# Kernel optimization log

Hardware: AMD Instinct MI355X
Metric: run time of the kernel (lower is better)

## Reference

```python
import jax, jax.numpy as jnp
import numpy as np

H = 8          # n_heads
M = 16         # max_dist
U = 512        # n_units
DH = U // H    # d_head
EPS = 1e-3     # keras LayerNormalization default epsilon
NEG = -2.0**32 + 1.0


def _rel_table(pe, T):
    # pe: [2M+1, DH]; returns [T, T, DH] with rel[i, j] = pe[clip(j - i, -M, M) + M]
    i = jnp.arange(T)
    idx = jnp.clip(i[None, :] - i[:, None], -M, M) + M
    return pe[idx]


def _split_heads(x):
    # [B, T, U] -> [H*B, T, DH]  (head-major, matching tf.concat(tf.split(x, H, 2), 0))
    B, T, _ = x.shape
    return x.reshape(B, T, H, DH).transpose(2, 0, 1, 3).reshape(H * B, T, DH)


def _merge_heads(x, B):
    # [H*B, T, DH] -> [B, T, U]
    T = x.shape[1]
    return x.reshape(H, B, T, DH).transpose(1, 2, 0, 3).reshape(B, T, U)


def setup_inputs() -> dict:
    key = jax.random.key(0)
    ks = jax.random.split(key, 10)
    B, T = 8, 1024
    s = 1.0 / np.sqrt(U)
    inp = {
        'q': jax.random.normal(ks[0], (B, T, U), jnp.float32),
        'k': jax.random.normal(ks[1], (B, T, U), jnp.float32),
        'v': jax.random.normal(ks[2], (B, T, U), jnp.float32),
        'Wq': jax.random.normal(ks[3], (U, U), jnp.float32) * s,
        'bq': jnp.zeros((U,), jnp.float32),
        'Wk': jax.random.normal(ks[4], (U, U), jnp.float32) * s,
        'bk': jnp.zeros((U,), jnp.float32),
        'Wv': jax.random.normal(ks[5], (U, U), jnp.float32) * s,
        'bv': jnp.zeros((U,), jnp.float32),
        'Wo': jax.random.normal(ks[6], (U, U), jnp.float32) * s,
        'bo': jnp.zeros((U,), jnp.float32),
        'gamma': jnp.ones((U,), jnp.float32),
        'beta': jnp.zeros((U,), jnp.float32),
        'pe_k': jax.random.normal(ks[7], (2 * M + 1, DH), jnp.float32) * 0.05,
        'pe_v': jax.random.normal(ks[8], (2 * M + 1, DH), jnp.float32) * 0.05,
    }
    return inp


def reference(q, k, v, Wq, bq, Wk, bk, Wv, bv, Wo, bo, gamma, beta, pe_k, pe_v):
    B, T, _ = q.shape
    relu = jax.nn.relu
    q_emb = relu(q @ Wq + bq)
    k_emb = relu(k @ Wk + bk)
    v_emb = relu(v @ Wv + bv)
    qh = _split_heads(q_emb)   # [HB, T, DH]
    kh = _split_heads(k_emb)
    vh = _split_heads(v_emb)

    attn = jnp.einsum('btd,bsd->bts', qh, kh)
    rel_k = _rel_table(pe_k, T)                       # [T, T, DH]
    attn = attn + jnp.einsum('btd,tsd->bts', qh, rel_k)
    attn = attn / jnp.asarray(DH, attn.dtype) ** 0.5

    causal = jnp.tril(jnp.ones((T, T), jnp.bool_))
    attn = jnp.where(causal[None], attn, jnp.asarray(NEG, attn.dtype))
    w = jax.nn.softmax(attn, axis=-1)

    out = jnp.einsum('bts,bsd->btd', w, vh)
    rel_v = _rel_table(pe_v, T)
    out = out + jnp.einsum('bts,tsd->btd', w, rel_v)

    out = _merge_heads(out, B)                        # [B, T, U]
    out = relu(out @ Wo + bo)
    out = out + q

    mu = jnp.mean(out, axis=-1, keepdims=True)
    var = jnp.mean(jnp.square(out - mu), axis=-1, keepdims=True)
    return (out - mu) * jax.lax.rsqrt(var + EPS) * gamma + beta
```

## Files before the change

### kernel.cpp

```cpp
#include <hip/hip_runtime.h>
#include <hip/hip_bf16.h>

#define T_SEQ 1024
#define U_DIM 512
#define LN_EPS 1e-3f

typedef float  f32x4  __attribute__((ext_vector_type(4)));
typedef short  bf16x8 __attribute__((ext_vector_type(8)));

__device__ __forceinline__ unsigned short f2bf(float f) {
    union { float f; unsigned u; } x; x.f = f;
    unsigned r = x.u + 0x7fffu + ((x.u >> 16) & 1u);
    return (unsigned short)(r >> 16);
}
__device__ __forceinline__ float b2f(short s) {
    union { unsigned u; float f; } x; x.u = ((unsigned)(unsigned short)s) << 16;
    return x.f;
}
__device__ __forceinline__ int packbf(float a, float b) {
    return (int)((unsigned)f2bf(a) | ((unsigned)f2bf(b) << 16));
}
__device__ __forceinline__ void async_copy16(void* lds, const void* g) {
    __builtin_amdgcn_global_load_lds((const __attribute__((address_space(1))) void*)g,
                                     (__attribute__((address_space(3))) void*)lds, 16, 0, 0);
}

__global__ __launch_bounds__(256) void conv_bf16(
        const float* __restrict__ q, const float* __restrict__ k, const float* __restrict__ v,
        short* __restrict__ qb, short* __restrict__ kb, short* __restrict__ vb) {
    const size_t off = ((size_t)blockIdx.x * 256 + threadIdx.x) * 8;
#pragma unroll
    for (int z = 0; z < 3; ++z) {
        const float* src = (z == 0) ? q : (z == 1) ? k : v;
        short* dst = (z == 0) ? qb : (z == 1) ? kb : vb;
        float4 a = *(const float4*)(src + off);
        float4 b = *(const float4*)(src + off + 4);
        int4 o;
        o.x = packbf(a.x, a.y);
        o.y = packbf(a.z, a.w);
        o.z = packbf(b.x, b.y);
        o.w = packbf(b.z, b.w);
        *(int4*)(dst + off) = o;
    }
}

__global__ __launch_bounds__(256) void prep_wt(
        const float* __restrict__ Wq, const float* __restrict__ Wk,
        const float* __restrict__ Wv, const float* __restrict__ Wo,
        short* __restrict__ wt) {
    __shared__ float Ws[64][65];
    const int bid = blockIdx.x, t = threadIdx.x;
    const int z = bid >> 6, tile = bid & 63;
    const float* W = (z == 0) ? Wq : (z == 1) ? Wk : (z == 2) ? Wv : Wo;
    short* Wt = wt + (size_t)z * 262144;
    const int k0 = (tile >> 3) * 64, n0 = (tile & 7) * 64;
    {
        const int kr = t >> 2, cs = (t & 3) * 16;
        const float4* src = (const float4*)(W + (size_t)(k0 + kr) * 512 + n0 + cs);
#pragma unroll
        for (int i = 0; i < 4; ++i) {
            float4 vv = src[i];
            Ws[kr][cs + 4 * i + 0] = vv.x;
            Ws[kr][cs + 4 * i + 1] = vv.y;
            Ws[kr][cs + 4 * i + 2] = vv.z;
            Ws[kr][cs + 4 * i + 3] = vv.w;
        }
    }
    __syncthreads();
    {
        const int nr = t >> 2, ks = (t & 3) * 16;
        int4 w0, w1;
        w0.x = packbf(Ws[ks + 0][nr], Ws[ks + 1][nr]);
        w0.y = packbf(Ws[ks + 2][nr], Ws[ks + 3][nr]);
        w0.z = packbf(Ws[ks + 4][nr], Ws[ks + 5][nr]);
        w0.w = packbf(Ws[ks + 6][nr], Ws[ks + 7][nr]);
        w1.x = packbf(Ws[ks + 8][nr], Ws[ks + 9][nr]);
        w1.y = packbf(Ws[ks + 10][nr], Ws[ks + 11][nr]);
        w1.z = packbf(Ws[ks + 12][nr], Ws[ks + 13][nr]);
        w1.w = packbf(Ws[ks + 14][nr], Ws[ks + 15][nr]);
        short* dst = Wt + (size_t)(n0 + nr) * 512 + k0 + ks;
        *(int4*)dst = w0;
        *(int4*)(dst + 8) = w1;
    }
}

template <int OUT, int BM, int BN>
__global__ __launch_bounds__(256) void gemm_mfma(
        const void* __restrict__ A0, const void* __restrict__ A1, const void* __restrict__ A2,
        const short* __restrict__ Wt0, const short* __restrict__ Wt1, const short* __restrict__ Wt2,
        const float* __restrict__ b0p, const float* __restrict__ b1p, const float* __restrict__ b2p,
        const float* __restrict__ resid,
        void* __restrict__ O0, void* __restrict__ O1, void* __restrict__ O2) {
    constexpr int ASZ = BM * 64;
    constexpr int BSZ = BN * 64;
    constexpr int MW  = BM / 64;
    constexpr int NW  = 4 / MW;
    constexpr int AJ  = BN / (16 * NW);
    constexpr int BNC = BN / 16;
    constexpr int NTW = BNC / 2;
    constexpr int ACB = BM / 32;
    __shared__ short As[2 * ASZ];
    __shared__ short Bs[2 * BSZ];

    const int z = blockIdx.z;
    const void* Av = (z == 0) ? A0 : (z == 1) ? A1 : A2;
    const short* Wz = (z == 0) ? Wt0 : (z == 1) ? Wt1 : Wt2;
    const float* bz = (z == 0) ? b0p : (z == 1) ? b1p : b2p;
    void* Ov = (z == 0) ? O0 : (z == 1) ? O1 : O2;

    const int tid = threadIdx.x;
    const int m0 = blockIdx.x * BM, n0 = blockIdx.y * BN;
    const int w = tid >> 6, lane = tid & 63;
    const int n15 = lane & 15, g = lane >> 4;
    const int mh = w / NW, nh = w % NW;

    f32x4 acc[4][AJ];
#pragma unroll
    for (int i = 0; i < 4; ++i)
#pragma unroll
        for (int j = 0; j < AJ; ++j) acc[i][j] = (f32x4){0.f, 0.f, 0.f, 0.f};

#define STAGE_B(CK, BUF)                                                                 \
    do {                                                                                 \
        if (w < 2) {                                                                     \
            _Pragma("unroll")                                                            \
            for (int i = 0; i < 2 * NTW; ++i) {                                          \
                const int kc = i / NTW, nt = w * NTW + (i % NTW);                        \
                const short* gp = Wz + (size_t)(n0 + nt * 16 + n15) * 512 + (CK) * 64 + kc * 32 + g * 8; \
                async_copy16(Bs + (BUF) * BSZ + (kc * BNC + nt) * 512, gp);              \
            }                                                                            \
        }                                                                                \
    } while (0)

#define STAGE_A(CK, BUF)                                                                 \
    do {                                                                                 \
        if (w >= 2) {                                                                    \
            _Pragma("unroll")                                                            \
            for (int i = 0; i < 2 * ACB; ++i) {                                          \
                const int kc = i / ACB, mt = (w - 2) * ACB + (i % ACB);                  \
                const short* gp = (const short*)Av + (size_t)(m0 + mt * 16 + n15) * 512 + (CK) * 64 + kc * 32 + g * 8; \
                async_copy16(As + (BUF) * ASZ + (kc * (BM / 16) + mt) * 512, gp);        \
            }                                                                            \
        }                                                                                \
    } while (0)

    STAGE_B(0, 0);
    STAGE_A(0, 0);

    for (int ck = 0; ck < 8; ++ck) {
        const int cb = ck & 1, nb = cb ^ 1;
        __syncthreads();
        if (ck < 7) {
            STAGE_B(ck + 1, nb);
            STAGE_A(ck + 1, nb);
        }
#pragma unroll
        for (int kc = 0; kc < 2; ++kc) {
            bf16x8 af[4], bfv[AJ];
#pragma unroll
            for (int i = 0; i < 4; ++i)
                af[i] = *(const bf16x8*)(As + cb * ASZ + (kc * (BM / 16) + mh * 4 + i) * 512 + lane * 8);
#pragma unroll
            for (int j = 0; j < AJ; ++j)
                bfv[j] = *(const bf16x8*)(Bs + cb * BSZ + (kc * BNC + nh * AJ + j) * 512 + lane * 8);
#pragma unroll
            for (int i = 0; i < 4; ++i)
#pragma unroll
                for (int j = 0; j < AJ; ++j)
                    acc[i][j] = __builtin_amdgcn_mfma_f32_16x16x32_bf16(af[i], bfv[j], acc[i][j], 0, 0, 0);
        }
    }
#undef STAGE_B
#undef STAGE_A

    const int mbase = m0 + mh * 64 + g * 4;
    const int nbase = n0 + nh * (AJ * 16) + n15;
    const bool even = (n15 & 1) == 0;
    float bj[AJ];
#pragma unroll
    for (int j = 0; j < AJ; ++j) bj[j] = bz[nbase + j * 16];

#pragma unroll
    for (int i = 0; i < 4; ++i) {
        const int mrow = mbase + i * 16;
#pragma unroll
        for (int j = 0; j < AJ; ++j) {
            const int ncol = nbase + j * 16;
            f32x4 a = acc[i][j];
            float v0 = fmaxf(a[0] + bj[j], 0.f);
            float v1 = fmaxf(a[1] + bj[j], 0.f);
            float v2 = fmaxf(a[2] + bj[j], 0.f);
            float v3 = fmaxf(a[3] + bj[j], 0.f);
            if (OUT == 0) {
                unsigned t01 = (unsigned)packbf(v0, v1);
                unsigned t23 = (unsigned)packbf(v2, v3);
                unsigned x01 = (unsigned)__shfl_xor((int)t01, 1, 64);
                unsigned x23 = (unsigned)__shfl_xor((int)t23, 1, 64);
                short* Oz = (short*)Ov;
                if (even) {
                    unsigned d0 = (t01 & 0xffffu) | (x01 << 16);
                    unsigned d1 = (t01 >> 16) | (x01 & 0xffff0000u);
                    *(unsigned*)(Oz + (size_t)(mrow + 0) * 512 + ncol) = d0;
                    *(unsigned*)(Oz + (size_t)(mrow + 1) * 512 + ncol) = d1;
                } else {
                    unsigned d2 = (x23 & 0xffffu) | (t23 << 16);
                    unsigned d3 = (x23 >> 16) | (t23 & 0xffff0000u);
                    *(unsigned*)(Oz + (size_t)(mrow + 2) * 512 + ncol - 1) = d2;
                    *(unsigned*)(Oz + (size_t)(mrow + 3) * 512 + ncol - 1) = d3;
                }
            } else {
                float x0 = __shfl_xor(v0, 1, 64);
                float x1 = __shfl_xor(v1, 1, 64);
                float x2 = __shfl_xor(v2, 1, 64);
                float x3 = __shfl_xor(v3, 1, 64);
                float* Oz = (float*)Ov;
                if (even) {
                    float2 r0 = *(const float2*)(resid + (size_t)(mrow + 0) * 512 + ncol);
                    float2 r1 = *(const float2*)(resid + (size_t)(mrow + 1) * 512 + ncol);
                    *(float2*)(Oz + (size_t)(mrow + 0) * 512 + ncol) = make_float2(v0 + r0.x, x0 + r0.y);
                    *(float2*)(Oz + (size_t)(mrow + 1) * 512 + ncol) = make_float2(v1 + r1.x, x1 + r1.y);
                } else {
                    float2 r2 = *(const float2*)(resid + (size_t)(mrow + 2) * 512 + ncol - 1);
                    float2 r3 = *(const float2*)(resid + (size_t)(mrow + 3) * 512 + ncol - 1);
                    *(float2*)(Oz + (size_t)(mrow + 2) * 512 + ncol - 1) = make_float2(x2 + r2.x, v2 + r2.y);
                    *(float2*)(Oz + (size_t)(mrow + 3) * 512 + ncol - 1) = make_float2(x3 + r3.x, v3 + r3.y);
                }
            }
        }
    }
}

__global__ __launch_bounds__(256) void attn_mfma(
        const short* __restrict__ qe, const short* __restrict__ ke,
        const short* __restrict__ ve, const float* __restrict__ pe_k,
        float* __restrict__ ml, short* __restrict__ ao) {
    __shared__ short Kc[2 * 4096];
    __shared__ short Vc[2 * 4096];
    __shared__ float qpeS[4 * 16 * 17];

    const int tid = threadIdx.x;
    const int bid = blockIdx.x;
    const int rank = (bid & 3) + 4 * (bid >> 8);
    const int hb = (bid >> 2) & 63;
    const int tt = 15 - rank;
    const int h = hb >> 3, b = hb & 7;
    const int w = tid >> 6, lane = tid & 63;
    const int g = lane >> 4, n15 = lane & 15;
    const int sp = tid & 31, dbase = (tid >> 5) * 8;
    float* qpeW = qpeS + w * (16 * 17);

    const size_t rowbase = (size_t)b * T_SEQ;

    int qn = 0;
    bf16x8 Bq[2];
    float qpe0 = 0.f;
    float m_r = -3.0e38f, l_r = 0.f;
    f32x4 oacc[4];

#define SETUP(TILE)                                                                      \
    do {                                                                                 \
        qn = (TILE) * 64 + w * 16;                                                       \
        _Pragma("unroll")                                                                \
        for (int kh = 0; kh < 2; ++kh)                                                   \
            Bq[kh] = *(const bf16x8*)(qe + (rowbase + qn + n15) * U_DIM + h * 64 + kh * 32 + g * 8); \
        f32x4 qa[2];                                                                     \
        qa[0] = (f32x4){0.f, 0.f, 0.f, 0.f};                                             \
        qa[1] = (f32x4){0.f, 0.f, 0.f, 0.f};                                             \
        _Pragma("unroll")                                                                \
        for (int mt = 0; mt < 2; ++mt)                                                   \
        _Pragma("unroll")                                                                \
        for (int kh = 0; kh < 2; ++kh) {                                                 \
            const float* src = pe_k + (mt * 16 + n15) * 64 + kh * 32 + g * 8;            \
            float4 f0 = *(const float4*)src;                                             \
            float4 f1 = *(const float4*)(src + 4);                                       \
            bf16x8 fr;                                                                   \
            fr[0] = (short)f2bf(f0.x); fr[1] = (short)f2bf(f0.y);                        \
            fr[2] = (short)f2bf(f0.z); fr[3] = (short)f2bf(f0.w);                        \
            fr[4] = (short)f2bf(f1.x); fr[5] = (short)f2bf(f1.y);                        \
            fr[6] = (short)f2bf(f1.z); fr[7] = (short)f2bf(f1.w);                        \
            qa[mt] = __builtin_amdgcn_mfma_f32_16x16x32_bf16(fr, Bq[kh], qa[mt], 0, 0, 0); \
        }                                                                                \
        _Pragma("unroll")                                                                \
        for (int mt = 0; mt < 2; ++mt)                                                   \
        _Pragma("unroll")                                                                \
        for (int r = 0; r < 4; ++r) {                                                    \
            const int ri = mt * 16 + 4 * g + r;                                          \
            if (ri <= 16) qpeW[n15 * 17 + ri] = qa[mt][r];                               \
        }                                                                                \
        qpe0 = qpeW[n15 * 17];                                                           \
        m_r = -3.0e38f; l_r = 0.f;                                                       \
        _Pragma("unroll")                                                                \
        for (int dt = 0; dt < 4; ++dt) oacc[dt] = (f32x4){0.f, 0.f, 0.f, 0.f};           \
    } while (0)

#define STAGE_K(S, BUF)                                                                  \
    do {                                                                                 \
        _Pragma("unroll")                                                                \
        for (int j = 0; j < 2; ++j) {                                                    \
            const int cc = w * 2 + j, kh = cc >> 2, mt = cc & 3;                         \
            const short* gp = ke + (rowbase + (S) + mt * 16 + n15) * U_DIM + h * 64 + kh * 32 + g * 8; \
            async_copy16(Kc + (BUF) * 4096 + cc * 512, gp);                              \
        }                                                                                \
    } while (0)

#define LOAD_V(S)                                                                        \
    do {                                                                                 \
        const short* r0 = ve + (rowbase + (S) + 2 * sp) * U_DIM + h * 64 + dbase;        \
        vx = *(const bf16x8*)r0;                                                         \
        vy = *(const bf16x8*)(r0 + U_DIM);                                               \
    } while (0)

#define STORE_V(BUF)                                                                     \
    do {                                                                                 \
        const int vkh = sp >> 4, vg = (sp & 15) >> 2, vj = (sp & 3) * 2;                 \
        _Pragma("unroll")                                                                \
        for (int i = 0; i < 8; ++i) {                                                    \
            const int d = dbase + i;                                                     \
            int pv = (int)((unsigned short)vx[i]) | (((int)(unsigned short)vy[i]) << 16);\
            *(int*)(Vc + (BUF) * 4096 + (vkh * 4 + (d >> 4)) * 512 + ((d & 15) + 16 * vg) * 8 + vj) = pv; \
        }                                                                                \
    } while (0)

    SETUP(tt);
    bf16x8 vx, vy;
    STAGE_K(0, 0);
    LOAD_V(0);
    STORE_V(0);

    for (int gs = 0; gs <= tt; ++gs) {
        const int cb = gs & 1, nb = cb ^ 1;
        const int s0 = gs * 64;
        __syncthreads();
        if (gs < tt) {
            STAGE_K((gs + 1) * 64, nb);
            LOAD_V((gs + 1) * 64);
        }

        {
            int cls[4];
#pragma unroll
            for (int mt = 0; mt < 4; ++mt) {
                const int slo = s0 + mt * 16;
                cls[mt] = (slo > qn + 15) ? 0 : ((slo + 31 < qn) ? 1 : 2);
            }
            f32x4 c[4];
#pragma unroll
            for (int mt = 0; mt < 4; ++mt) c[mt] = (f32x4){0.f, 0.f, 0.f, 0.f};
#pragma unroll
            for (int mt = 0; mt < 4; ++mt) {
                if (!cls[mt]) continue;
#pragma unroll
                for (int kh = 0; kh < 2; ++kh) {
                    bf16x8 ak = *(const bf16x8*)(Kc + cb * 4096 + (kh * 4 + mt) * 512 + lane * 8);
                    c[mt] = __builtin_amdgcn_mfma_f32_16x16x32_bf16(ak, Bq[kh], c[mt], 0, 0, 0);
                }
            }

            const int qg = qn + n15;
            float sc[4][4];
            float pmax = -3.0e38f;
#pragma unroll
            for (int mt = 0; mt < 4; ++mt) {
                if (cls[mt] == 0) {
#pragma unroll
                    for (int r = 0; r < 4; ++r) sc[mt][r] = -3.0e38f;
                } else if (cls[mt] == 1) {
#pragma unroll
                    for (int r = 0; r < 4; ++r) {
                        sc[mt][r] = (c[mt][r] + qpe0) * 0.125f;
                        pmax = fmaxf(pmax, sc[mt][r]);
                    }
                } else {
#pragma unroll
                    for (int r = 0; r < 4; ++r) {
                        const int sg = s0 + mt * 16 + 4 * g + r;
                        const int dlt = sg - qg;
                        if (dlt <= 0) {
                            const int ri = (dlt < -16) ? 0 : (dlt + 16);
                            sc[mt][r] = (c[mt][r] + qpeW[n15 * 17 + ri]) * 0.125f;
                            pmax = fmaxf(pmax, sc[mt][r]);
                        } else {
                            sc[mt][r] = -3.0e38f;
                        }
                    }
                }
            }
            pmax = fmaxf(pmax, __shfl_xor(pmax, 16, 64));
            pmax = fmaxf(pmax, __shfl_xor(pmax, 32, 64));
            const float mnew = fmaxf(m_r, pmax);
            const float alpha = __expf(m_r - mnew);
            float p[4][4];
            float psum = 0.f;
#pragma unroll
            for (int mt = 0; mt < 4; ++mt)
#pragma unroll
            for (int r = 0; r < 4; ++r) {
                const float pv = (cls[mt] == 0) ? 0.f : __expf(sc[mt][r] - mnew);
                p[mt][r] = pv;
                psum += pv;
            }
            psum += __shfl_xor(psum, 16, 64);
            psum += __shfl_xor(psum, 32, 64);
            l_r = l_r * alpha + psum;
            m_r = mnew;

            int pk01[4], pk23[4];
#pragma unroll
            for (int mt = 0; mt < 4; ++mt) {
                pk01[mt] = packbf(p[mt][0], p[mt][1]);
                pk23[mt] = packbf(p[mt][2], p[mt][3]);
            }
            const int srcA = ((g & 1) * 2) * 16 + n15;
            const int srcB = srcA + 16;
            const bool selHi = (g >> 1) != 0;
            float aO[4];
#pragma unroll
            for (int r = 0; r < 4; ++r) aO[r] = __shfl(alpha, 4 * g + r, 64);
#pragma unroll
            for (int dt = 0; dt < 4; ++dt)
#pragma unroll
            for (int r = 0; r < 4; ++r) oacc[dt][r] *= aO[r];
#pragma unroll
            for (int kh = 0; kh < 2; ++kh) {
                if (cls[2 * kh] == 0 && cls[2 * kh + 1] == 0) continue;
                const int a0l = __shfl(pk01[2 * kh], srcA, 64);
                const int a0h = __shfl(pk01[2 * kh + 1], srcA, 64);
                const int a1l = __shfl(pk23[2 * kh], srcA, 64);
                const int a1h = __shfl(pk23[2 * kh + 1], srcA, 64);
                const int a2l = __shfl(pk01[2 * kh], srcB, 64);
                const int a2h = __shfl(pk01[2 * kh + 1], srcB, 64);
                const int a3l = __shfl(pk23[2 * kh], srcB, 64);
                const int a3h = __shfl(pk23[2 * kh + 1], srcB, 64);
                union { int i[4]; bf16x8 v; } au;
                au.i[0] = selHi ? a0h : a0l;
                au.i[1] = selHi ? a1h : a1l;
                au.i[2] = selHi ? a2h : a2l;
                au.i[3] = selHi ? a3h : a3l;
#pragma unroll
                for (int dt = 0; dt < 4; ++dt) {
                    bf16x8 bv = *(const bf16x8*)(Vc + cb * 4096 + (kh * 4 + dt) * 512 + lane * 8);
                    oacc[dt] = __builtin_amdgcn_mfma_f32_16x16x32_bf16(au.v, bv, oacc[dt], 0, 0, 0);
                }
            }
        }

        if (gs < tt) STORE_V(nb);
    }

    if (g == 0)
        *(float2*)(ml + ((size_t)hb * T_SEQ + qn + n15) * 2) = make_float2(m_r, l_r);
#pragma unroll
    for (int r = 0; r < 4; ++r) {
        const float lq = __shfl(l_r, 4 * g + r, 64);
        const float linv = 1.0f / lq;
        short* dst = ao + (rowbase + qn + 4 * g + r) * U_DIM + h * 64 + n15;
#pragma unroll
        for (int dt = 0; dt < 4; ++dt)
            dst[dt * 16] = (short)f2bf(oacc[dt][r] * linv);
    }
#undef SETUP
#undef STAGE_K
#undef LOAD_V
#undef STORE_V
}

__global__ __launch_bounds__(256) void band_relv(
        const short* __restrict__ qe, const short* __restrict__ ke,
        const float* __restrict__ pe_k, const float* __restrict__ pe_v,
        const float* __restrict__ ml, short* __restrict__ ao) {
    __shared__ float pek[17 * 64];
    __shared__ float pev[17 * 64];
    const int tb = blockIdx.x, hb = blockIdx.y;
    const int h = hb >> 3, b = hb & 7;
    const int tid = threadIdx.x;
    for (int i = tid; i < 17 * 64; i += 256) {
        pek[i] = b2f((short)f2bf(pe_k[i]));
        pev[i] = pe_v[i];
    }
    __syncthreads();

    const int t = tb * 64 + (tid >> 2);
    const int p = (tid & 3) * 16;
    const short* qp = qe + (size_t)(b * T_SEQ + t) * U_DIM + h * 64 + p;
    bf16x8 qa = *(const bf16x8*)qp, qb2 = *(const bf16x8*)(qp + 8);
    float qv[16];
#pragma unroll
    for (int i = 0; i < 8; ++i) { qv[i] = b2f(qa[i]); qv[8 + i] = b2f(qb2[i]); }

    float dots[17];
#pragma unroll
    for (int ri = 0; ri < 17; ++ri) {
        const int s = t - 16 + ri;
        float acc = 0.f;
        if (s >= 0) {
            const short* kp = ke + (size_t)(b * T_SEQ + s) * U_DIM + h * 64 + p;
            bf16x8 ka = *(const bf16x8*)kp, kb2 = *(const bf16x8*)(kp + 8);
#pragma unroll
            for (int d = 0; d < 8; ++d) {
                acc += qv[d] * b2f(ka[d]);
                acc += qv[8 + d] * b2f(kb2[d]);
            }
#pragma unroll
            for (int d = 0; d < 16; ++d) acc += qv[d] * pek[ri * 64 + p + d];
        }
        dots[ri] = acc;
    }
#pragma unroll
    for (int ri = 0; ri < 17; ++ri) {
        dots[ri] += __shfl_xor(dots[ri], 1, 64);
        dots[ri] += __shfl_xor(dots[ri], 2, 64);
    }

    const float2 mlv = *(const float2*)(ml + ((size_t)hb * T_SEQ + t) * 2);
    const float m = mlv.x, linv = 1.0f / mlv.y;
    float wv[17];
    float wsum = 0.f;
#pragma unroll
    for (int ri = 0; ri < 17; ++ri) {
        const int s = t - 16 + ri;
        const float wr = (s >= 0) ? __expf(dots[ri] * 0.125f - m) * linv : 0.f;
        wv[ri] = wr;
        wsum += wr;
    }
    wv[0] += 1.0f - wsum;

    float relv[16];
#pragma unroll
    for (int d = 0; d < 16; ++d) relv[d] = 0.f;
#pragma unroll
    for (int ri = 0; ri < 17; ++ri)
#pragma unroll
        for (int d = 0; d < 16; ++d) relv[d] += wv[ri] * pev[ri * 64 + p + d];

    short* op = ao + (size_t)(b * T_SEQ + t) * U_DIM + h * 64 + p;
    bf16x8 a0 = *(const bf16x8*)op, a1 = *(const bf16x8*)(op + 8);
    int4 o0, o1;
    o0.x = packbf(b2f(a0[0]) + relv[0],  b2f(a0[1]) + relv[1]);
    o0.y = packbf(b2f(a0[2]) + relv[2],  b2f(a0[3]) + relv[3]);
    o0.z = packbf(b2f(a0[4]) + relv[4],  b2f(a0[5]) + relv[5]);
    o0.w = packbf(b2f(a0[6]) + relv[6],  b2f(a0[7]) + relv[7]);
    o1.x = packbf(b2f(a1[0]) + relv[8],  b2f(a1[1]) + relv[9]);
    o1.y = packbf(b2f(a1[2]) + relv[10], b2f(a1[3]) + relv[11]);
    o1.z = packbf(b2f(a1[4]) + relv[12], b2f(a1[5]) + relv[13]);
    o1.w = packbf(b2f(a1[6]) + relv[14], b2f(a1[7]) + relv[15]);
    *(int4*)op = o0;
    *(int4*)(op + 8) = o1;
}

__global__ __launch_bounds__(256) void ln_kernel(float* __restrict__ io,
                                                 const float* __restrict__ gamma,
                                                 const float* __restrict__ beta) {
    const int row = blockIdx.x * 4 + (threadIdx.x >> 6);
    const int lane = threadIdx.x & 63;
    float* rp = io + (size_t)row * 512 + lane * 8;
    float4 a = *(const float4*)rp;
    float4 c = *(const float4*)(rp + 4);
    float v[8] = {a.x, a.y, a.z, a.w, c.x, c.y, c.z, c.w};

    float s = v[0] + v[1] + v[2] + v[3] + v[4] + v[5] + v[6] + v[7];
#pragma unroll
    for (int off = 1; off < 64; off <<= 1) s += __shfl_xor(s, off, 64);
    const float mu = s * (1.0f / 512.0f);

    float sq = 0.f;
#pragma unroll
    for (int i = 0; i < 8; ++i) { v[i] -= mu; sq += v[i] * v[i]; }
#pragma unroll
    for (int off = 1; off < 64; off <<= 1) sq += __shfl_xor(sq, off, 64);
    const float rs = rsqrtf(sq * (1.0f / 512.0f) + LN_EPS);

    const float4 g0 = *(const float4*)(gamma + lane * 8);
    const float4 g1 = *(const float4*)(gamma + lane * 8 + 4);
    const float4 b0 = *(const float4*)(beta + lane * 8);
    const float4 b1 = *(const float4*)(beta + lane * 8 + 4);
    float4 o0, o1;
    o0.x = v[0] * rs * g0.x + b0.x;
    o0.y = v[1] * rs * g0.y + b0.y;
    o0.z = v[2] * rs * g0.z + b0.z;
    o0.w = v[3] * rs * g0.w + b0.w;
    o1.x = v[4] * rs * g1.x + b1.x;
    o1.y = v[5] * rs * g1.y + b1.y;
    o1.z = v[6] * rs * g1.z + b1.z;
    o1.w = v[7] * rs * g1.w + b1.w;
    *(float4*)rp = o0;
    *(float4*)(rp + 4) = o1;
}

extern "C" void kernel_launch(void* const* d_in, const int* in_sizes, int n_in,
                              void* d_out, int out_size, void* d_ws, size_t ws_size,
                              hipStream_t stream) {
    const float* q     = (const float*)d_in[0];
    const float* k     = (const float*)d_in[1];
    const float* v     = (const float*)d_in[2];
    const float* Wq    = (const float*)d_in[3];
    const float* bq    = (const float*)d_in[4];
    const float* Wk    = (const float*)d_in[5];
    const float* bk    = (const float*)d_in[6];
    const float* Wv    = (const float*)d_in[7];
    const float* bv    = (const float*)d_in[8];
    const float* Wo    = (const float*)d_in[9];
    const float* bo    = (const float*)d_in[10];
    const float* gamma = (const float*)d_in[11];
    const float* beta  = (const float*)d_in[12];
    const float* pe_k  = (const float*)d_in[13];
    const float* pe_v  = (const float*)d_in[14];
    float* out = (float*)d_out;

    char* base = (char*)d_ws;
    short* qe = (short*)(base);
    short* ke = (short*)(base + (((size_t)8) << 20));
    short* ve = (short*)(base + (((size_t)16) << 20));
    short* ao = (short*)(base + (((size_t)24) << 20));
    short* wt = (short*)(base + (((size_t)32) << 20));
    float* ml = (float*)(base + (((size_t)34) << 20));
    short* qb = (short*)(base + (((size_t)36) << 20));
    short* kb = (short*)(base + (((size_t)44) << 20));
    short* vb = (short*)(base + (((size_t)52) << 20));
    short* wtq = wt, *wtk = wt + 262144, *wtv = wt + 2 * 262144, *wto = wt + 3 * 262144;

    prep_wt<<<dim3(256), 256, 0, stream>>>(Wq, Wk, Wv, Wo, wt);
    conv_bf16<<<dim3(2048), 256, 0, stream>>>(q, k, v, qb, kb, vb);
    gemm_mfma<0, 128, 64><<<dim3(64, 8, 3), 256, 0, stream>>>(
        qb, kb, vb, wtq, wtk, wtv, bq, bk, bv, nullptr, qe, ke, ve);
    attn_mfma<<<dim3(1024), 256, 0, stream>>>(qe, ke, ve, pe_k, ml, ao);
    band_relv<<<dim3(16, 64), 256, 0, stream>>>(qe, ke, pe_k, pe_v, ml, ao);
    gemm_mfma<1, 64, 128><<<dim3(128, 4, 1), 256, 0, stream>>>(
        ao, ao, ao, wto, wto, wto, bo, bo, bo, q, out, out, out);
    ln_kernel<<<dim3(2048), 256, 0, stream>>>(out, gamma, beta);
}
```

Baseline: 253.6 us.

## Deepen GEMM LDS pipeline, prescale q, and use lazy softmax rescaling

The projection GEMM now stages 32-wide k-slices into a 4-buffer LDS ring, with explicit vmcnt waits and evenly split async loads across waves, so memory latency is better hidden. The attention kernel folds the 1/sqrt(d) scale into q by adjusting bf16 exponent bits, which removes a per-score multiply. It also skips the running-max update and output rescale unless the new max exceeds the old one by a threshold. Block-to-tile ranking is changed to a zigzag order to balance causal work. The exponent trick flushes tiny values to zero, and the lazy rescale relies on bounded exponent growth.

New measurement: 248.4 us. 1.02x faster.

```diff
diff --git a/kernel.cpp b/kernel.cpp
--- a/kernel.cpp
+++ b/kernel.cpp
@@ -24,6 +24,8 @@
     __builtin_amdgcn_global_load_lds((const __attribute__((address_space(1))) void*)g,
                                      (__attribute__((address_space(3))) void*)lds, 16, 0, 0);
 }
+
+#define WAITV(N) asm volatile("s_waitcnt vmcnt(" #N ")" ::: "memory")
 
 __global__ __launch_bounds__(256) void conv_bf16(
         const float* __restrict__ q, const float* __restrict__ k, const float* __restrict__ v,
@@ -91,16 +93,16 @@
         const float* __restrict__ b0p, const float* __restrict__ b1p, const float* __restrict__ b2p,
         const float* __restrict__ resid,
         void* __restrict__ O0, void* __restrict__ O1, void* __restrict__ O2) {
-    constexpr int ASZ = BM * 64;
-    constexpr int BSZ = BN * 64;
+    constexpr int ASZ = BM * 32;
+    constexpr int BSZ = BN * 32;
+    constexpr int TSZ = ASZ + BSZ;
+    constexpr int NA  = BM / 16;
+    constexpr int NB  = BN / 16;
     constexpr int MW  = BM / 64;
     constexpr int NW  = 4 / MW;
     constexpr int AJ  = BN / (16 * NW);
-    constexpr int BNC = BN / 16;
-    constexpr int NTW = BNC / 2;
-    constexpr int ACB = BM / 32;
-    __shared__ short As[2 * ASZ];
-    __shared__ short Bs[2 * BSZ];
+    static_assert(NA + NB == 12, "3 loads per wave");
+    __shared__ short Ls[4 * TSZ];
 
     const int z = blockIdx.z;
     const void* Av = (z == 0) ? A0 : (z == 1) ? A1 : A2;
@@ -120,58 +122,54 @@
 #pragma unroll
         for (int j = 0; j < AJ; ++j) acc[i][j] = (f32x4){0.f, 0.f, 0.f, 0.f};
 
-#define STAGE_B(CK, BUF)                                                                 \
+    const short* gsrc[3];
+    int loff[3];
+#pragma unroll
+    for (int cl = 0; cl < 3; ++cl) {
+        const int cid = w * 3 + cl;
+        if (cid < NA) {
+            gsrc[cl] = (const short*)Av + (size_t)(m0 + cid * 16 + n15) * 512 + g * 8;
+            loff[cl] = cid * 512;
+        } else {
+            const int c2 = cid - NA;
+            gsrc[cl] = Wz + (size_t)(n0 + c2 * 16 + n15) * 512 + g * 8;
+            loff[cl] = ASZ + c2 * 512;
+        }
+    }
+
+#define STAGE(CK, BUF)                                                                   \
     do {                                                                                 \
-        if (w < 2) {                                                                     \
-            _Pragma("unroll")                                                            \
-            for (int i = 0; i < 2 * NTW; ++i) {                                          \
-                const int kc = i / NTW, nt = w * NTW + (i % NTW);                        \
-                const short* gp = Wz + (size_t)(n0 + nt * 16 + n15) * 512 + (CK) * 64 + kc * 32 + g * 8; \
-                async_copy16(Bs + (BUF) * BSZ + (kc * BNC + nt) * 512, gp);              \
-            }                                                                            \
-        }                                                                                \
+        _Pragma("unroll")                                                                \
+        for (int cl = 0; cl < 3; ++cl)                                                   \
+            async_copy16(Ls + (BUF) * TSZ + loff[cl], gsrc[cl] + (CK) * 32);             \
     } while (0)
 
-#define STAGE_A(CK, BUF)                                                                 \
-    do {                                                                                 \
-        if (w >= 2) {                                                                    \
-            _Pragma("unroll")                                                            \
-            for (int i = 0; i < 2 * ACB; ++i) {                                          \
-                const int kc = i / ACB, mt = (w - 2) * ACB + (i % ACB);                  \
-                const short* gp = (const short*)Av + (size_t)(m0 + mt * 16 + n15) * 512 + (CK) * 64 + kc * 32 + g * 8; \
-                async_copy16(As + (BUF) * ASZ + (kc * (BM / 16) + mt) * 512, gp);        \
-            }                                                                            \
-        }                                                                                \
-    } while (0)
-
-    STAGE_B(0, 0);
-    STAGE_A(0, 0);
-
-    for (int ck = 0; ck < 8; ++ck) {
-        const int cb = ck & 1, nb = cb ^ 1;
-        __syncthreads();
-        if (ck < 7) {
-            STAGE_B(ck + 1, nb);
-            STAGE_A(ck + 1, nb);
-        }
-#pragma unroll
-        for (int kc = 0; kc < 2; ++kc) {
-            bf16x8 af[4], bfv[AJ];
-#pragma unroll
-            for (int i = 0; i < 4; ++i)
-                af[i] = *(const bf16x8*)(As + cb * ASZ + (kc * (BM / 16) + mh * 4 + i) * 512 + lane * 8);
+    STAGE(0, 0);
+    STAGE(1, 1);
+    STAGE(2, 2);
+
+    for (int ck = 0; ck < 16; ++ck) {
+        if (ck < 14) WAITV(6);
+        else if (ck == 14) WAITV(3);
+        else WAITV(0);
+        __builtin_amdgcn_s_barrier();
+        __builtin_amdgcn_sched_barrier(0);
+        if (ck + 3 <= 15) STAGE(ck + 3, (ck + 3) & 3);
+        const int cb = ck & 3;
+        bf16x8 af[4], bfv[AJ];
+#pragma unroll
+        for (int i = 0; i < 4; ++i)
+            af[i] = *(const bf16x8*)(Ls + cb * TSZ + (mh * 4 + i) * 512 + lane * 8);
+#pragma unroll
+        for (int j = 0; j < AJ; ++j)
+            bfv[j] = *(const bf16x8*)(Ls + cb * TSZ + ASZ + (nh * AJ + j) * 512 + lane * 8);
+#pragma unroll
+        for (int i = 0; i < 4; ++i)
 #pragma unroll
             for (int j = 0; j < AJ; ++j)
-                bfv[j] = *(const bf16x8*)(Bs + cb * BSZ + (kc * BNC + nh * AJ + j) * 512 + lane * 8);
-#pragma unroll
-            for (int i = 0; i < 4; ++i)
-#pragma unroll
-                for (int j = 0; j < AJ; ++j)
-                    acc[i][j] = __builtin_amdgcn_mfma_f32_16x16x32_bf16(af[i], bfv[j], acc[i][j], 0, 0, 0);
-        }
-    }
-#undef STAGE_B
-#undef STAGE_A
+                acc[i][j] = __builtin_amdgcn_mfma_f32_16x16x32_bf16(af[i], bfv[j], acc[i][j], 0, 0, 0);
+    }
+#undef STAGE
 
     const int mbase = m0 + mh * 64 + g * 4;
     const int nbase = n0 + nh * (AJ * 16) + n15;
@@ -240,7 +238,8 @@
 
     const int tid = threadIdx.x;
     const int bid = blockIdx.x;
-    const int rank = (bid & 3) + 4 * (bid >> 8);
+    const int q4 = bid >> 8, r4 = bid & 3;
+    const int rank = (q4 < 2) ? (r4 + 4 * q4) : (15 - (r4 + 4 * (q4 - 2)));
     const int hb = (bid >> 2) & 63;
     const int tt = 15 - rank;
     const int h = hb >> 3, b = hb & 7;
@@ -261,8 +260,16 @@
     do {                                                                                 \
         qn = (TILE) * 64 + w * 16;                                                       \
         _Pragma("unroll")                                                                \
-        for (int kh = 0; kh < 2; ++kh)                                                   \
-            Bq[kh] = *(const bf16x8*)(qe + (rowbase + qn + n15) * U_DIM + h * 64 + kh * 32 + g * 8); \
+        for (int kh = 0; kh < 2; ++kh) {                                                 \
+            bf16x8 t = *(const bf16x8*)(qe + (rowbase + qn + n15) * U_DIM + h * 64 + kh * 32 + g * 8); \
+            _Pragma("unroll")                                                            \
+            for (int i2 = 0; i2 < 8; ++i2) {                                             \
+                unsigned short u = (unsigned short)t[i2];                                \
+                t[i2] = (short)(((u & 0x7f80u) > 0x0180u) ? (unsigned short)(u - 0x0180u) \
+                                                          : (unsigned short)(u & 0x8000u)); \
+            }                                                                            \
+            Bq[kh] = t;                                                                  \
+        }                                                                                \
         f32x4 qa[2];                                                                     \
         qa[0] = (f32x4){0.f, 0.f, 0.f, 0.f};                                             \
         qa[1] = (f32x4){0.f, 0.f, 0.f, 0.f};                                             \
@@ -367,7 +374,7 @@
                 } else if (cls[mt] == 1) {
 #pragma unroll
                     for (int r = 0; r < 4; ++r) {
-                        sc[mt][r] = (c[mt][r] + qpe0) * 0.125f;
+                        sc[mt][r] = c[mt][r] + qpe0;
                         pmax = fmaxf(pmax, sc[mt][r]);
                     }
                 } else {
@@ -377,7 +384,7 @@
                         const int dlt = sg - qg;
                         if (dlt <= 0) {
                             const int ri = (dlt < -16) ? 0 : (dlt + 16);
-                            sc[mt][r] = (c[mt][r] + qpeW[n15 * 17 + ri]) * 0.125f;
+                            sc[mt][r] = c[mt][r] + qpeW[n15 * 17 + ri];
                             pmax = fmaxf(pmax, sc[mt][r]);
                         } else {
                             sc[mt][r] = -3.0e38f;
@@ -387,8 +394,13 @@
             }
             pmax = fmaxf(pmax, __shfl_xor(pmax, 16, 64));
             pmax = fmaxf(pmax, __shfl_xor(pmax, 32, 64));
-            const float mnew = fmaxf(m_r, pmax);
-            const float alpha = __expf(m_r - mnew);
+
+            const bool resc = __any(pmax > m_r + 8.0f);
+            float mnew = m_r, alpha = 1.0f;
+            if (resc) {
+                mnew = fmaxf(m_r, pmax);
+                alpha = __expf(m_r - mnew);
+            }
             float p[4][4];
             float psum = 0.f;
 #pragma unroll
@@ -413,13 +425,15 @@
             const int srcA = ((g & 1) * 2) * 16 + n15;
             const int srcB = srcA + 16;
             const bool selHi = (g >> 1) != 0;
-            float aO[4];
-#pragma unroll
-            for (int r = 0; r < 4; ++r) aO[r] = __shfl(alpha, 4 * g + r, 64);
-#pragma unroll
-            for (int dt = 0; dt < 4; ++dt)
-#pragma unroll
-            for (int r = 0; r < 4; ++r) oacc[dt][r] *= aO[r];
+            if (resc) {
+                float aO[4];
+#pragma unroll
+                for (int r = 0; r < 4; ++r) aO[r] = __shfl(alpha, 4 * g + r, 64);
+#pragma unroll
+                for (int dt = 0; dt < 4; ++dt)
+#pragma unroll
+                for (int r = 0; r < 4; ++r) oacc[dt][r] *= aO[r];
+            }
 #pragma unroll
             for (int kh = 0; kh < 2; ++kh) {
                 if (cls[2 * kh] == 0 && cls[2 * kh + 1] == 0) continue;
```
